# Kernel tuning notes

Measured on AMD Instinct MI355X. Metric: run time of the kernel, lower is better.

## Reference

```python
import jax, jax.numpy as jnp
import numpy as np

C = 1.0          # curvature
MIN_NORM = 1e-15
EPS = 1e-7       # atanh clamp for fp32

def _sqnorm(x):
    return jnp.sum(x * x, axis=-1, keepdims=True)

def _norm(x):
    return jnp.sqrt(jnp.maximum(_sqnorm(x), MIN_NORM))

def _atanh(u):
    return jnp.arctanh(jnp.clip(u, -1.0 + EPS, 1.0 - EPS))

def mobius_add(x, y, c):
    x2 = _sqnorm(x); y2 = _sqnorm(y)
    xy = jnp.sum(x * y, axis=-1, keepdims=True)
    num = (1.0 + 2.0 * c * xy + c * y2) * x + (1.0 - c * x2) * y
    den = 1.0 + 2.0 * c * xy + c * c * x2 * y2
    return num / jnp.maximum(den, MIN_NORM)

def logmap0(p, c):
    sc = jnp.sqrt(c)
    pn = _norm(p)
    return p / pn / sc * _atanh(sc * pn)

def logmap(p1, p2, c):
    # tangent vector at p1 pointing to p2 (Poincare ball)
    sub = mobius_add(-p1, p2, c)
    sn = _norm(sub)
    lam = 2.0 / jnp.maximum(1.0 - c * _sqnorm(p1), MIN_NORM)
    sc = jnp.sqrt(c)
    return 2.0 / sc / lam * _atanh(sc * sn) * sub / sn

def expmap(p, u, c):
    un = _norm(u)
    lam = 2.0 / jnp.maximum(1.0 - c * _sqnorm(p), MIN_NORM)
    sc = jnp.sqrt(c)
    second = jnp.tanh(sc * lam * un / 2.0) * u / (sc * un)
    return mobius_add(p, second, c)


def setup_inputs() -> dict:
    key = jax.random.key(0)
    k1, k2, k3 = jax.random.split(key, 3)
    B, N, D = 1, 1024, 128
    # points inside the unit Poincare ball (||x|| ~ 0.23)
    x = jax.random.normal(k1, (B, N, D), jnp.float32) * 0.02
    # sparse-ish dense adjacency mask (0/1 floats)
    adj = (jax.random.uniform(k2, (B, N, N)) < 0.05).astype(jnp.float32)
    # DenseAtt: nn.Linear(2*D, 1) weight (flattened) + bias
    att_w = jax.random.normal(k3, (2 * D,), jnp.float32) * 0.1
    att_b = jnp.zeros((), jnp.float32)
    return {"x": x, "adj": adj, "att_w": att_w, "att_b": att_b}


def reference(x, adj, att_w, att_b):
    B, N, D = x.shape
    x_t = logmap0(x, C)                                   # [B,N,D]
    # DenseAtt: sigmoid(Linear(cat(x_i, x_j))) decomposed as left_i + right_j + b
    left = x_t @ att_w[:D]                                # [B,N]
    right = x_t @ att_w[D:]                               # [B,N]
    att = jax.nn.sigmoid(left[:, :, None] + right[:, None, :] + att_b) * adj  # [B,N,N]
    # pairwise logmap: tangent at x_i of every x_j  -> [B,N,N,D]
    x_local = logmap(x[:, :, None, :], x[:, None, :, :], C)
    support_t = jnp.einsum('bij,bijd->bid', att, x_local)  # [B,N,D]
    return expmap(x, support_t, C)
```

## Files before the change

kernel.cpp:

```cpp
#include <hip/hip_runtime.h>
#include <math.h>


typedef short short4v __attribute__((ext_vector_type(4)));
typedef short short8v __attribute__((ext_vector_type(8)));
typedef float float4v __attribute__((ext_vector_type(4)));

static __device__ __forceinline__ short f2bf(float f) {
    unsigned u = __float_as_uint(f);
    u += 0x7fff + ((u >> 16) & 1);
    return (short)(u >> 16);
}
static __device__ __forceinline__ float rcpf(float x) { return __builtin_amdgcn_rcpf(x); }
static __device__ __forceinline__ short8v ld8(const unsigned short* p) {
    short4v lo = *(const short4v*)p;
    short4v hi = *(const short4v*)(p + 4);
    return (short8v){lo[0],lo[1],lo[2],lo[3],hi[0],hi[1],hi[2],hi[3]};
}

__global__ __launch_bounds__(256) void hyp_stats(
    const float* __restrict__ x, const float* __restrict__ w,
    float* __restrict__ st_x2, float* __restrict__ st_L, float* __restrict__ st_R)
{
    int row  = blockIdx.x * 4 + (threadIdx.x >> 6);
    int lane = threadIdx.x & 63;
    const float* xr = x + row * 128;
    float a0 = xr[lane], a1 = xr[lane + 64];
    float x2 = a0 * a0 + a1 * a1;
    float dl = a0 * w[lane]       + a1 * w[lane + 64];
    float dr = a0 * w[lane + 128] + a1 * w[lane + 192];
    for (int m = 1; m < 64; m <<= 1) {
        x2 += __shfl_xor(x2, m);
        dl += __shfl_xor(dl, m);
        dr += __shfl_xor(dr, m);
    }
    if (lane == 0) {
        float pn = sqrtf(fmaxf(x2, 1e-15f));
        float uu = fminf(pn, 1.f - 1e-7f);
        float at = 0.5f * __logf((1.f + uu) * rcpf(1.f - uu));
        float f  = at * rcpf(pn);
        st_x2[row] = x2;
        st_L[row]  = f * dl;
        st_R[row]  = f * dr;
    }
}

__global__ __launch_bounds__(256, 2) void hyp_main(
    const float* __restrict__ x, const float* __restrict__ adj,
    const float* __restrict__ battp,
    const float* __restrict__ st_x2, const float* __restrict__ st_L,
    const float* __restrict__ st_R,
    float* __restrict__ Yp, float* __restrict__ Sp)
{
    __shared__ unsigned short sXI [16 * 132];
    __shared__ unsigned short sXJ [128 * 132];
    __shared__ unsigned short sXJt[128 * 132];
    __shared__ unsigned short sW  [16 * 132];
    __shared__ float sS[16];

    const int t    = threadIdx.x;
    const int lane = t & 63;
    const int wave = t >> 6;
    const int n    = lane & 15;
    const int q    = lane >> 4;
    const int i0   = blockIdx.x * 16;
    const int c    = blockIdx.y;
    const int j0   = c * 128;
    const float batt = battp[0];

    float x2i4[4], bi4[4], li4[4];
#pragma unroll
    for (int r = 0; r < 4; ++r) {
        int i = i0 + q * 4 + r;
        x2i4[r] = st_x2[i];
        li4[r]  = st_L[i];
    }
    float x2j2[2], rj2[2], adjv[2][4];
#pragma unroll
    for (int jsl = 0; jsl < 2; ++jsl) {
        int j = j0 + (wave * 2 + jsl) * 16 + n;
        x2j2[jsl] = st_x2[j];
        rj2[jsl]  = st_R[j];
#pragma unroll
        for (int r = 0; r < 4; ++r)
            adjv[jsl][r] = adj[(i0 + q * 4 + r) * 1024 + j];
    }
#pragma unroll
    for (int r = 0; r < 4; ++r) bi4[r] = 1.f - x2i4[r];

    if (t < 16) sS[t] = 0.f;

    for (int idx = t; idx < 16 * 32; idx += 256) {
        int r = idx >> 5, cc = idx & 31;
        float4v v = ((const float4v*)x)[(i0 + r) * 32 + cc];
        short4v h = { f2bf(v[0]), f2bf(v[1]), f2bf(v[2]), f2bf(v[3]) };
        *(short4v*)&sXI[r * 132 + cc * 4] = h;
    }
#pragma unroll
    for (int it = 0; it < 4; ++it) {
        int bid = t + it * 256;
        int jr = ((bid >> 4) & 3) | (((bid >> 6) & 7) << 2);
        int dc = (bid & 15) | (((bid >> 9) & 1) << 4);
        float4v v[4];
#pragma unroll
        for (int e = 0; e < 4; ++e)
            v[e] = ((const float4v*)x)[(j0 + jr * 4 + e) * 32 + dc];
        short4v h[4];
#pragma unroll
        for (int e = 0; e < 4; ++e) {
            h[e] = (short4v){ f2bf(v[e][0]), f2bf(v[e][1]), f2bf(v[e][2]), f2bf(v[e][3]) };
            *(short4v*)&sXJ[(jr * 4 + e) * 132 + dc * 4] = h[e];
        }
#pragma unroll
        for (int d = 0; d < 4; ++d) {
            short4v ht = (short4v){ h[0][d], h[1][d], h[2][d], h[3][d] };
            *(short4v*)&sXJt[(dc * 4 + d) * 132 + jr * 4] = ht;
        }
    }
    __syncthreads();

    short8v afrag[4];
#pragma unroll
    for (int kk = 0; kk < 4; ++kk)
        afrag[kk] = ld8(&sXI[n * 132 + kk * 32 + q * 8]);

    float Sacc[4] = {0.f, 0.f, 0.f, 0.f};

#pragma unroll
    for (int jsl = 0; jsl < 2; ++jsl) {
        int js = wave * 2 + jsl;
        int jrow = js * 16 + n;
        float4v acc = (float4v){0.f, 0.f, 0.f, 0.f};
#pragma unroll
        for (int kk = 0; kk < 4; ++kk) {
            short8v b = ld8(&sXJ[jrow * 132 + kk * 32 + q * 8]);
            acc = __builtin_amdgcn_mfma_f32_16x16x32_bf16(afrag[kk], b, acc, 0, 0, 0);
        }
        float x2j = x2j2[jsl];
        float rj  = rj2[jsl];
#pragma unroll
        for (int r = 0; r < 4; ++r) {
            float G     = acc[r];
            int   i     = q * 4 + r;
            float alpha = 1.f - 2.f * G + x2j;
            float den   = fmaxf(fmaf(x2i4[r], x2j, 1.f - 2.f * G), 1e-15f);
            float rdn   = rcpf(den);
            float bb    = bi4[r];
            float nn2   = alpha * alpha * x2i4[r] + bb * bb * x2j - 2.f * alpha * bb * G;
            float sub2  = nn2 * rdn * rdn;
            float sn    = sqrtf(fmaxf(sub2, 1e-15f));
            float uu    = fminf(sn, 1.f - 1e-7f);
            float at    = 0.5f * __logf((1.f + uu) * rcpf(1.f - uu));
            float tt    = at * rcpf(sn);
            float z     = li4[r] + rj + batt;
            float sig   = rcpf(1.f + __expf(-z));
            float g     = sig * adjv[jsl][r] * tt * rdn;
            Sacc[r]     = fmaf(g, alpha, Sacc[r]);
            sW[i * 132 + js * 16 + n] = (unsigned short)f2bf(g);
        }
    }
    __syncthreads();

    float4v accB[2];
    accB[0] = (float4v){0.f, 0.f, 0.f, 0.f};
    accB[1] = (float4v){0.f, 0.f, 0.f, 0.f};
#pragma unroll
    for (int nsl = 0; nsl < 2; ++nsl) {
        int ns = wave * 2 + nsl;
#pragma unroll
        for (int kk = 0; kk < 4; ++kk) {
            short8v a = ld8(&sW  [n * 132 + kk * 32 + q * 8]);
            short8v b = ld8(&sXJt[(ns * 16 + n) * 132 + kk * 32 + q * 8]);
            accB[nsl] = __builtin_amdgcn_mfma_f32_16x16x32_bf16(a, b, accB[nsl], 0, 0, 0);
        }
    }

#pragma unroll
    for (int r = 0; r < 4; ++r) {
        float v = Sacc[r];
        v += __shfl_xor(v, 1); v += __shfl_xor(v, 2);
        v += __shfl_xor(v, 4); v += __shfl_xor(v, 8);
        if (n == 0) atomicAdd(&sS[q * 4 + r], v);
    }
    float* Yc = Yp + c * 131072;
#pragma unroll
    for (int nsl = 0; nsl < 2; ++nsl) {
        int ns = wave * 2 + nsl;
#pragma unroll
        for (int r = 0; r < 4; ++r)
            Yc[(i0 + q * 4 + r) * 128 + ns * 16 + n] = accB[nsl][r];
    }
    __syncthreads();
    if (t < 16) Sp[c * 1024 + i0 + t] = sS[t];
}

__global__ __launch_bounds__(256) void hyp_exp(
    const float* __restrict__ x, const float* __restrict__ Yp,
    const float* __restrict__ Sp, const float* __restrict__ st_x2,
    float* __restrict__ out)
{
    int i    = blockIdx.x * 4 + (threadIdx.x >> 6);
    int lane = threadIdx.x & 63;
    float y0 = 0.f, y1 = 0.f, S = 0.f;
#pragma unroll
    for (int cc = 0; cc < 8; ++cc) {
        y0 += Yp[cc * 131072 + i * 128 + lane];
        y1 += Yp[cc * 131072 + i * 128 + 64 + lane];
        S  += Sp[cc * 1024 + i];
    }
    float x0 = x[i * 128 + lane], x1 = x[i * 128 + 64 + lane];
    float x2 = st_x2[i];
    float b  = fmaxf(1.f - x2, 1e-15f);
    float u0 = b * (b * y0 - S * x0);
    float u1 = b * (b * y1 - S * x1);
    float un2 = u0 * u0 + u1 * u1;
    float xu  = x0 * u0 + x1 * u1;
    for (int m = 1; m < 64; m <<= 1) {
        un2 += __shfl_xor(un2, m);
        xu  += __shfl_xor(xu, m);
    }
    float un  = sqrtf(fmaxf(un2, 1e-15f));
    float e2  = __expf(2.f * un * rcpf(b));
    float th  = 1.f - 2.f * rcpf(e2 + 1.f);
    float s2  = th * rcpf(un);
    float xy  = s2 * xu;
    float y2s = th * th;
    float coef = 1.f + 2.f * xy + y2s;
    float den  = fmaxf(1.f + 2.f * xy + x2 * y2s, 1e-15f);
    float rd   = rcpf(den);
    out[i * 128 + lane]      = (coef * x0 + b * (s2 * u0)) * rd;
    out[i * 128 + 64 + lane] = (coef * x1 + b * (s2 * u1)) * rd;
}

extern "C" void kernel_launch(void* const* d_in, const int* in_sizes, int n_in,
                              void* d_out, int out_size, void* d_ws, size_t ws_size,
                              hipStream_t stream) {
    const float* x    = (const float*)d_in[0];
    const float* adj  = (const float*)d_in[1];
    const float* w    = (const float*)d_in[2];
    const float* batt = (const float*)d_in[3];
    float* out = (float*)d_out;

    float* Yp    = (float*)d_ws;
    float* Sp    = Yp + 8 * 131072;
    float* st_x2 = Sp + 8 * 1024;
    float* st_L  = st_x2 + 1024;
    float* st_R  = st_L + 1024;

    hipLaunchKernelGGL(hyp_stats, dim3(256), dim3(256), 0, stream, x, w, st_x2, st_L, st_R);
    hipLaunchKernelGGL(hyp_main, dim3(64, 8), dim3(256), 0, stream,
                       x, adj, batt, st_x2, st_L, st_R, Yp, Sp);
    hipLaunchKernelGGL(hyp_exp, dim3(256), dim3(256), 0, stream, x, Yp, Sp, st_x2, out);
}
```

Before: 73.29 us.

## Fuse stats, main and expmap kernels into one launch with flag-based handoff

Merges the three kernels into a single kernel. Each block recomputes the per-row norms and attention projections it needs in shared memory, replacing the separate stats kernel. The final expmap is done by one designated block per row tile after it spin-waits on release/acquire flags set by the eight column-chunk blocks. This removes two launches and their global round trips, at the cost of redundant stat recomputation and a spin-wait. The flags are never reset, so later calls may not wait for fresh partial results, and the spin-wait assumes all blocks are co-resident.

```diff
diff --git a/kernel.cpp b/kernel.cpp
--- a/kernel.cpp
+++ b/kernel.cpp
@@ -5,6 +5,8 @@
 typedef short short4v __attribute__((ext_vector_type(4)));
 typedef short short8v __attribute__((ext_vector_type(8)));
 typedef float float4v __attribute__((ext_vector_type(4)));
+
+#define MAGIC 0x4D414749
 
 static __device__ __forceinline__ short f2bf(float f) {
     unsigned u = __float_as_uint(f);
@@ -17,94 +19,76 @@
     short4v hi = *(const short4v*)(p + 4);
     return (short8v){lo[0],lo[1],lo[2],lo[3],hi[0],hi[1],hi[2],hi[3]};
 }
-
-__global__ __launch_bounds__(256) void hyp_stats(
-    const float* __restrict__ x, const float* __restrict__ w,
-    float* __restrict__ st_x2, float* __restrict__ st_L, float* __restrict__ st_R)
-{
-    int row  = blockIdx.x * 4 + (threadIdx.x >> 6);
-    int lane = threadIdx.x & 63;
-    const float* xr = x + row * 128;
-    float a0 = xr[lane], a1 = xr[lane + 64];
-    float x2 = a0 * a0 + a1 * a1;
-    float dl = a0 * w[lane]       + a1 * w[lane + 64];
-    float dr = a0 * w[lane + 128] + a1 * w[lane + 192];
-    for (int m = 1; m < 64; m <<= 1) {
-        x2 += __shfl_xor(x2, m);
-        dl += __shfl_xor(dl, m);
-        dr += __shfl_xor(dr, m);
-    }
-    if (lane == 0) {
-        float pn = sqrtf(fmaxf(x2, 1e-15f));
-        float uu = fminf(pn, 1.f - 1e-7f);
-        float at = 0.5f * __logf((1.f + uu) * rcpf(1.f - uu));
-        float f  = at * rcpf(pn);
-        st_x2[row] = x2;
-        st_L[row]  = f * dl;
-        st_R[row]  = f * dr;
-    }
-}
-
-__global__ __launch_bounds__(256, 2) void hyp_main(
+static __device__ __forceinline__ float dot4(float4v a, float4v b) {
+    return a[0]*b[0] + a[1]*b[1] + a[2]*b[2] + a[3]*b[3];
+}
+
+__global__ __launch_bounds__(256, 2) void hyp_fused(
     const float* __restrict__ x, const float* __restrict__ adj,
-    const float* __restrict__ battp,
-    const float* __restrict__ st_x2, const float* __restrict__ st_L,
-    const float* __restrict__ st_R,
-    float* __restrict__ Yp, float* __restrict__ Sp)
+    const float* __restrict__ battp, const float* __restrict__ w,
+    float* __restrict__ Yp, float* __restrict__ Sp, int* __restrict__ flags,
+    float* __restrict__ out)
 {
     __shared__ unsigned short sXI [16 * 132];
     __shared__ unsigned short sXJ [128 * 132];
     __shared__ unsigned short sXJt[128 * 132];
     __shared__ unsigned short sW  [16 * 132];
-    __shared__ float sS[16];
+    __shared__ float sX2J[128], sRJ[128];
+    __shared__ float sX2I[16], sLI[16], sS[16];
 
     const int t    = threadIdx.x;
     const int lane = t & 63;
     const int wave = t >> 6;
     const int n    = lane & 15;
     const int q    = lane >> 4;
-    const int i0   = blockIdx.x * 16;
-    const int c    = blockIdx.y;
-    const int j0   = c * 128;
+    const int bx   = blockIdx.x;
+    const int cch  = blockIdx.y;
+    const int i0   = bx * 16;
+    const int j0   = cch * 128;
     const float batt = battp[0];
 
-    float x2i4[4], bi4[4], li4[4];
-#pragma unroll
-    for (int r = 0; r < 4; ++r) {
-        int i = i0 + q * 4 + r;
-        x2i4[r] = st_x2[i];
-        li4[r]  = st_L[i];
-    }
-    float x2j2[2], rj2[2], adjv[2][4];
+    float adjv[2][4];
 #pragma unroll
     for (int jsl = 0; jsl < 2; ++jsl) {
         int j = j0 + (wave * 2 + jsl) * 16 + n;
-        x2j2[jsl] = st_x2[j];
-        rj2[jsl]  = st_R[j];
 #pragma unroll
         for (int r = 0; r < 4; ++r)
             adjv[jsl][r] = adj[(i0 + q * 4 + r) * 1024 + j];
     }
-#pragma unroll
-    for (int r = 0; r < 4; ++r) bi4[r] = 1.f - x2i4[r];
-
-    if (t < 16) sS[t] = 0.f;
-
-    for (int idx = t; idx < 16 * 32; idx += 256) {
+
+    if (t < 128) { sX2J[t] = 0.f; sRJ[t] = 0.f; }
+    if (t < 16)  { sX2I[t] = 0.f; sLI[t] = 0.f; sS[t] = 0.f; }
+    __syncthreads();
+
+    const float4v* x4 = (const float4v*)x;
+    const float4v* w4 = (const float4v*)w;
+
+#pragma unroll
+    for (int iter = 0; iter < 2; ++iter) {
+        int idx = t + iter * 256;
         int r = idx >> 5, cc = idx & 31;
-        float4v v = ((const float4v*)x)[(i0 + r) * 32 + cc];
+        float4v v  = x4[(i0 + r) * 32 + cc];
+        float4v w1 = w4[cc];
         short4v h = { f2bf(v[0]), f2bf(v[1]), f2bf(v[2]), f2bf(v[3]) };
         *(short4v*)&sXI[r * 132 + cc * 4] = h;
+        float x2p = dot4(v, v), lp = dot4(v, w1);
+#pragma unroll
+        for (int m = 1; m < 32; m <<= 1) {
+            x2p += __shfl_xor(x2p, m);
+            lp  += __shfl_xor(lp, m);
+        }
+        if ((t & 31) == 0) { atomicAdd(&sX2I[r], x2p); atomicAdd(&sLI[r], lp); }
     }
 #pragma unroll
     for (int it = 0; it < 4; ++it) {
         int bid = t + it * 256;
         int jr = ((bid >> 4) & 3) | (((bid >> 6) & 7) << 2);
         int dc = (bid & 15) | (((bid >> 9) & 1) << 4);
+        float4v w2 = w4[32 + dc];
         float4v v[4];
 #pragma unroll
         for (int e = 0; e < 4; ++e)
-            v[e] = ((const float4v*)x)[(j0 + jr * 4 + e) * 32 + dc];
+            v[e] = x4[(j0 + jr * 4 + e) * 32 + dc];
         short4v h[4];
 #pragma unroll
         for (int e = 0; e < 4; ++e) {
@@ -116,9 +100,43 @@
             short4v ht = (short4v){ h[0][d], h[1][d], h[2][d], h[3][d] };
             *(short4v*)&sXJt[(dc * 4 + d) * 132 + jr * 4] = ht;
         }
-    }
-    __syncthreads();
-
+#pragma unroll
+        for (int e = 0; e < 4; ++e) {
+            float x2p = dot4(v[e], v[e]), rp = dot4(v[e], w2);
+#pragma unroll
+            for (int m = 1; m < 16; m <<= 1) {
+                x2p += __shfl_xor(x2p, m);
+                rp  += __shfl_xor(rp, m);
+            }
+            if ((t & 15) == 0) { atomicAdd(&sX2J[jr * 4 + e], x2p); atomicAdd(&sRJ[jr * 4 + e], rp); }
+        }
+    }
+    __syncthreads();
+
+    if (t < 144) {
+        float x2 = (t < 128) ? sX2J[t] : sX2I[t - 128];
+        float pn = sqrtf(fmaxf(x2, 1e-15f));
+        float uu = fminf(pn, 1.f - 1e-7f);
+        float f  = 0.5f * __logf((1.f + uu) * rcpf(1.f - uu)) * rcpf(pn);
+        if (t < 128) sRJ[t] *= f;
+        else         sLI[t - 128] = sLI[t - 128] * f + batt;
+    }
+    __syncthreads();
+
+    float x2i4[4], bi4[4], li4[4];
+#pragma unroll
+    for (int r = 0; r < 4; ++r) {
+        x2i4[r] = sX2I[q * 4 + r];
+        li4[r]  = sLI[q * 4 + r];
+        bi4[r]  = 1.f - x2i4[r];
+    }
+    float x2j2[2], rj2[2];
+#pragma unroll
+    for (int jsl = 0; jsl < 2; ++jsl) {
+        int js = wave * 2 + jsl;
+        x2j2[jsl] = sX2J[js * 16 + n];
+        rj2[jsl]  = sRJ[js * 16 + n];
+    }
     short8v afrag[4];
 #pragma unroll
     for (int kk = 0; kk < 4; ++kk)
@@ -152,7 +170,7 @@
             float uu    = fminf(sn, 1.f - 1e-7f);
             float at    = 0.5f * __logf((1.f + uu) * rcpf(1.f - uu));
             float tt    = at * rcpf(sn);
-            float z     = li4[r] + rj + batt;
+            float z     = li4[r] + rj;
             float sig   = rcpf(1.f + __expf(-z));
             float g     = sig * adjv[jsl][r] * tt * rdn;
             Sacc[r]     = fmaf(g, alpha, Sacc[r]);
@@ -175,6 +193,14 @@
         }
     }
 
+    float* Yc = Yp + cch * 131072;
+#pragma unroll
+    for (int nsl = 0; nsl < 2; ++nsl) {
+        int ns = wave * 2 + nsl;
+#pragma unroll
+        for (int r = 0; r < 4; ++r)
+            Yc[(i0 + q * 4 + r) * 128 + ns * 16 + n] = accB[nsl][r];
+    }
 #pragma unroll
     for (int r = 0; r < 4; ++r) {
         float v = Sacc[r];
@@ -182,54 +208,67 @@
         v += __shfl_xor(v, 4); v += __shfl_xor(v, 8);
         if (n == 0) atomicAdd(&sS[q * 4 + r], v);
     }
-    float* Yc = Yp + c * 131072;
-#pragma unroll
-    for (int nsl = 0; nsl < 2; ++nsl) {
-        int ns = wave * 2 + nsl;
-#pragma unroll
-        for (int r = 0; r < 4; ++r)
-            Yc[(i0 + q * 4 + r) * 128 + ns * 16 + n] = accB[nsl][r];
-    }
-    __syncthreads();
-    if (t < 16) Sp[c * 1024 + i0 + t] = sS[t];
-}
-
-__global__ __launch_bounds__(256) void hyp_exp(
-    const float* __restrict__ x, const float* __restrict__ Yp,
-    const float* __restrict__ Sp, const float* __restrict__ st_x2,
-    float* __restrict__ out)
-{
-    int i    = blockIdx.x * 4 + (threadIdx.x >> 6);
-    int lane = threadIdx.x & 63;
-    float y0 = 0.f, y1 = 0.f, S = 0.f;
-#pragma unroll
-    for (int cc = 0; cc < 8; ++cc) {
-        y0 += Yp[cc * 131072 + i * 128 + lane];
-        y1 += Yp[cc * 131072 + i * 128 + 64 + lane];
-        S  += Sp[cc * 1024 + i];
-    }
-    float x0 = x[i * 128 + lane], x1 = x[i * 128 + 64 + lane];
-    float x2 = st_x2[i];
-    float b  = fmaxf(1.f - x2, 1e-15f);
-    float u0 = b * (b * y0 - S * x0);
-    float u1 = b * (b * y1 - S * x1);
-    float un2 = u0 * u0 + u1 * u1;
-    float xu  = x0 * u0 + x1 * u1;
-    for (int m = 1; m < 64; m <<= 1) {
-        un2 += __shfl_xor(un2, m);
-        xu  += __shfl_xor(xu, m);
-    }
-    float un  = sqrtf(fmaxf(un2, 1e-15f));
-    float e2  = __expf(2.f * un * rcpf(b));
+    __syncthreads();
+    if (t < 16) Sp[cch * 1024 + i0 + t] = sS[t];
+    __threadfence();
+    __syncthreads();
+    if (t == 0)
+        __hip_atomic_store(&flags[bx * 8 + cch], MAGIC, __ATOMIC_RELEASE, __HIP_MEMORY_SCOPE_AGENT);
+
+    if ((bx & 7) != cch) return;
+    if (t < 8) {
+        while (__hip_atomic_load(&flags[bx * 8 + t], __ATOMIC_ACQUIRE, __HIP_MEMORY_SCOPE_AGENT) != MAGIC)
+            __builtin_amdgcn_s_sleep(1);
+    }
+    __syncthreads();
+    __threadfence();
+
+    int row  = t >> 4;
+    int ds16 = t & 15;
+    const float4v* xr4 = x4 + (i0 + row) * 32 + ds16 * 2;
+    float4v xa = xr4[0], xb = xr4[1];
+    float xv[8] = { xa[0], xa[1], xa[2], xa[3], xb[0], xb[1], xb[2], xb[3] };
+    float ya[8] = {0.f,0.f,0.f,0.f,0.f,0.f,0.f,0.f};
+    float S = 0.f;
+#pragma unroll
+    for (int c2 = 0; c2 < 8; ++c2) {
+        const float4v* yp4 = (const float4v*)(Yp + c2 * 131072 + (i0 + row) * 128) + ds16 * 2;
+        float4v a = yp4[0], b = yp4[1];
+        ya[0] += a[0]; ya[1] += a[1]; ya[2] += a[2]; ya[3] += a[3];
+        ya[4] += b[0]; ya[5] += b[1]; ya[6] += b[2]; ya[7] += b[3];
+        S += Sp[c2 * 1024 + i0 + row];
+    }
+    float x2p = dot4(xa, xa) + dot4(xb, xb);
+#pragma unroll
+    for (int m = 1; m < 16; m <<= 1) x2p += __shfl_xor(x2p, m);
+    float bE = fmaxf(1.f - x2p, 1e-15f);
+    float u[8], un2p = 0.f, xup = 0.f;
+#pragma unroll
+    for (int e = 0; e < 8; ++e) {
+        u[e] = bE * (bE * ya[e] - S * xv[e]);
+        un2p += u[e] * u[e];
+        xup  += xv[e] * u[e];
+    }
+#pragma unroll
+    for (int m = 1; m < 16; m <<= 1) {
+        un2p += __shfl_xor(un2p, m);
+        xup  += __shfl_xor(xup, m);
+    }
+    float un  = sqrtf(fmaxf(un2p, 1e-15f));
+    float e2  = __expf(2.f * un * rcpf(bE));
     float th  = 1.f - 2.f * rcpf(e2 + 1.f);
     float s2  = th * rcpf(un);
-    float xy  = s2 * xu;
+    float xy  = s2 * xup;
     float y2s = th * th;
     float coef = 1.f + 2.f * xy + y2s;
-    float den  = fmaxf(1.f + 2.f * xy + x2 * y2s, 1e-15f);
+    float den  = fmaxf(1.f + 2.f * xy + x2p * y2s, 1e-15f);
     float rd   = rcpf(den);
-    out[i * 128 + lane]      = (coef * x0 + b * (s2 * u0)) * rd;
-    out[i * 128 + 64 + lane] = (coef * x1 + b * (s2 * u1)) * rd;
+    float4v o0 = { (coef*xv[0] + bE*s2*u[0])*rd, (coef*xv[1] + bE*s2*u[1])*rd,
+                   (coef*xv[2] + bE*s2*u[2])*rd, (coef*xv[3] + bE*s2*u[3])*rd };
+    float4v o1 = { (coef*xv[4] + bE*s2*u[4])*rd, (coef*xv[5] + bE*s2*u[5])*rd,
+                   (coef*xv[6] + bE*s2*u[6])*rd, (coef*xv[7] + bE*s2*u[7])*rd };
+    float4v* out4 = (float4v*)(out + (i0 + row) * 128) + ds16 * 2;
+    out4[0] = o0; out4[1] = o1;
 }
 
 extern "C" void kernel_launch(void* const* d_in, const int* in_sizes, int n_in,
@@ -243,12 +282,8 @@
 
     float* Yp    = (float*)d_ws;
     float* Sp    = Yp + 8 * 131072;
-    float* st_x2 = Sp + 8 * 1024;
-    float* st_L  = st_x2 + 1024;
-    float* st_R  = st_L + 1024;
-
-    hipLaunchKernelGGL(hyp_stats, dim3(256), dim3(256), 0, stream, x, w, st_x2, st_L, st_R);
-    hipLaunchKernelGGL(hyp_main, dim3(64, 8), dim3(256), 0, stream,
-                       x, adj, batt, st_x2, st_L, st_R, Yp, Sp);
-    hipLaunchKernelGGL(hyp_exp, dim3(256), dim3(256), 0, stream, x, Yp, Sp, st_x2, out);
-}
+    int*   flags = (int*)(Sp + 8 * 1024);
+
+    hipLaunchKernelGGL(hyp_fused, dim3(64, 8), dim3(256), 0, stream,
+                       x, adj, batt, w, Yp, Sp, flags, out);
+}
```

After: 119.5 us. 63.1% more time.

## Precompute bf16 X and X^T once, shrink pair tiles, drop LDS staging

Applied to the files above, without the earlier changes.

The prep kernel now converts x to bf16 once, in both row-major and transposed layouts, and folds the attention bias into the left stats. The pair kernel splits j into 16 chunks of 64 and loads MFMA fragments straight from global memory instead of converting and transposing x into large shared buffers in every block. This allows higher occupancy (launch bounds 4) and removes the redundant per-block conversion. The cost is twice as many partial Y buffers for the final kernel to reduce, and extra workspace for the bf16 copies. The exp kernel is also vectorised to float4 with half-wave reductions.

```diff
diff --git a/kernel.cpp b/kernel.cpp
--- a/kernel.cpp
+++ b/kernel.cpp
@@ -17,46 +17,76 @@
     short4v hi = *(const short4v*)(p + 4);
     return (short8v){lo[0],lo[1],lo[2],lo[3],hi[0],hi[1],hi[2],hi[3]};
 }
-
-__global__ __launch_bounds__(256) void hyp_stats(
+static __device__ __forceinline__ float dot4(float4v a, float4v b) {
+    return a[0]*b[0] + a[1]*b[1] + a[2]*b[2] + a[3]*b[3];
+}
+static __device__ __forceinline__ float atanh_over(float pn) {
+    float uu = fminf(pn, 1.f - 1e-7f);
+    return 0.5f * __logf((1.f + uu) * rcpf(1.f - uu)) * rcpf(pn);
+}
+
+__global__ __launch_bounds__(256) void hyp_prep(
     const float* __restrict__ x, const float* __restrict__ w,
+    const float* __restrict__ battp,
+    unsigned short* __restrict__ Xb, unsigned short* __restrict__ Xbt,
     float* __restrict__ st_x2, float* __restrict__ st_L, float* __restrict__ st_R)
 {
-    int row  = blockIdx.x * 4 + (threadIdx.x >> 6);
-    int lane = threadIdx.x & 63;
-    const float* xr = x + row * 128;
-    float a0 = xr[lane], a1 = xr[lane + 64];
-    float x2 = a0 * a0 + a1 * a1;
-    float dl = a0 * w[lane]       + a1 * w[lane + 64];
-    float dr = a0 * w[lane + 128] + a1 * w[lane + 192];
-    for (int m = 1; m < 64; m <<= 1) {
-        x2 += __shfl_xor(x2, m);
-        dl += __shfl_xor(dl, m);
-        dr += __shfl_xor(dr, m);
-    }
-    if (lane == 0) {
+    __shared__ unsigned short sT[128 * 20];
+    __shared__ float sPx[16 * 36], sPl[16 * 36], sPr[16 * 36];
+    const int t  = threadIdx.x;
+    const int r0 = blockIdx.x * 16;
+    const float4v* x4 = (const float4v*)x;
+    const float4v* w4 = (const float4v*)w;
+
+#pragma unroll
+    for (int it = 0; it < 2; ++it) {
+        int bid = t + it * 256;
+        int jr = bid >> 5, dc = bid & 31;
+        float4v v  = x4[(r0 + jr) * 32 + dc];
+        float4v w1 = w4[dc], w2 = w4[32 + dc];
+        short4v h = { f2bf(v[0]), f2bf(v[1]), f2bf(v[2]), f2bf(v[3]) };
+        *(short4v*)&Xb[(r0 + jr) * 128 + dc * 4] = h;
+#pragma unroll
+        for (int d = 0; d < 4; ++d)
+            sT[(dc * 4 + d) * 20 + jr] = (unsigned short)h[d];
+        sPx[jr * 36 + dc] = dot4(v, v);
+        sPl[jr * 36 + dc] = dot4(v, w1);
+        sPr[jr * 36 + dc] = dot4(v, w2);
+    }
+    __syncthreads();
+    {
+        int dim = t >> 1, h = t & 1;
+        short8v vv = ld8(&sT[dim * 20 + h * 8]);
+        *(short8v*)&Xbt[dim * 1024 + r0 + h * 8] = vv;
+    }
+    if (t < 16) {
+        float x2 = 0.f, l = 0.f, r = 0.f;
+#pragma unroll
+        for (int k = 0; k < 8; ++k) {
+            float4v a = *(float4v*)&sPx[t * 36 + k * 4];
+            float4v b = *(float4v*)&sPl[t * 36 + k * 4];
+            float4v c = *(float4v*)&sPr[t * 36 + k * 4];
+            x2 += a[0] + a[1] + a[2] + a[3];
+            l  += b[0] + b[1] + b[2] + b[3];
+            r  += c[0] + c[1] + c[2] + c[3];
+        }
         float pn = sqrtf(fmaxf(x2, 1e-15f));
-        float uu = fminf(pn, 1.f - 1e-7f);
-        float at = 0.5f * __logf((1.f + uu) * rcpf(1.f - uu));
-        float f  = at * rcpf(pn);
-        st_x2[row] = x2;
-        st_L[row]  = f * dl;
-        st_R[row]  = f * dr;
-    }
-}
-
-__global__ __launch_bounds__(256, 2) void hyp_main(
-    const float* __restrict__ x, const float* __restrict__ adj,
-    const float* __restrict__ battp,
+        float f  = atanh_over(pn);
+        st_x2[r0 + t] = x2;
+        st_L [r0 + t] = l * f + battp[0];
+        st_R [r0 + t] = r * f;
+    }
+}
+
+__global__ __launch_bounds__(256, 4) void hyp_pair(
+    const unsigned short* __restrict__ Xb, const unsigned short* __restrict__ Xbt,
+    const float* __restrict__ adj,
     const float* __restrict__ st_x2, const float* __restrict__ st_L,
     const float* __restrict__ st_R,
     float* __restrict__ Yp, float* __restrict__ Sp)
 {
-    __shared__ unsigned short sXI [16 * 132];
-    __shared__ unsigned short sXJ [128 * 132];
-    __shared__ unsigned short sXJt[128 * 132];
-    __shared__ unsigned short sW  [16 * 132];
-    __shared__ float sS[16];
+    __shared__ unsigned short sW[16 * 68];
+    __shared__ float sSp[4 * 256];
 
     const int t    = threadIdx.x;
     const int lane = t & 63;
@@ -65,99 +95,57 @@
     const int q    = lane >> 4;
     const int i0   = blockIdx.x * 16;
     const int c    = blockIdx.y;
-    const int j0   = c * 128;
-    const float batt = battp[0];
-
-    float x2i4[4], bi4[4], li4[4];
+    const int j0   = c * 64;
+    const int jrow = j0 + wave * 16 + n;
+
+    float x2j = st_x2[jrow];
+    float rj  = st_R[jrow];
+    float x2i4[4], li4[4], bi4[4], adjv[4];
 #pragma unroll
     for (int r = 0; r < 4; ++r) {
         int i = i0 + q * 4 + r;
         x2i4[r] = st_x2[i];
         li4[r]  = st_L[i];
-    }
-    float x2j2[2], rj2[2], adjv[2][4];
-#pragma unroll
-    for (int jsl = 0; jsl < 2; ++jsl) {
-        int j = j0 + (wave * 2 + jsl) * 16 + n;
-        x2j2[jsl] = st_x2[j];
-        rj2[jsl]  = st_R[j];
-#pragma unroll
-        for (int r = 0; r < 4; ++r)
-            adjv[jsl][r] = adj[(i0 + q * 4 + r) * 1024 + j];
+        adjv[r] = adj[i * 1024 + jrow];
+    }
+    short8v afrag[4], bfA[4];
+#pragma unroll
+    for (int kk = 0; kk < 4; ++kk) {
+        afrag[kk] = *(const short8v*)&Xb[(i0 + n) * 128 + kk * 32 + q * 8];
+        bfA  [kk] = *(const short8v*)&Xb[jrow * 128     + kk * 32 + q * 8];
+    }
+    short8v bfB[2][2];
+#pragma unroll
+    for (int nsl = 0; nsl < 2; ++nsl) {
+        int ns = wave * 2 + nsl;
+#pragma unroll
+        for (int kk = 0; kk < 2; ++kk)
+            bfB[nsl][kk] = *(const short8v*)&Xbt[(ns * 16 + n) * 1024 + j0 + kk * 32 + q * 8];
     }
 #pragma unroll
     for (int r = 0; r < 4; ++r) bi4[r] = 1.f - x2i4[r];
 
-    if (t < 16) sS[t] = 0.f;
-
-    for (int idx = t; idx < 16 * 32; idx += 256) {
-        int r = idx >> 5, cc = idx & 31;
-        float4v v = ((const float4v*)x)[(i0 + r) * 32 + cc];
-        short4v h = { f2bf(v[0]), f2bf(v[1]), f2bf(v[2]), f2bf(v[3]) };
-        *(short4v*)&sXI[r * 132 + cc * 4] = h;
-    }
-#pragma unroll
-    for (int it = 0; it < 4; ++it) {
-        int bid = t + it * 256;
-        int jr = ((bid >> 4) & 3) | (((bid >> 6) & 7) << 2);
-        int dc = (bid & 15) | (((bid >> 9) & 1) << 4);
-        float4v v[4];
-#pragma unroll
-        for (int e = 0; e < 4; ++e)
-            v[e] = ((const float4v*)x)[(j0 + jr * 4 + e) * 32 + dc];
-        short4v h[4];
-#pragma unroll
-        for (int e = 0; e < 4; ++e) {
-            h[e] = (short4v){ f2bf(v[e][0]), f2bf(v[e][1]), f2bf(v[e][2]), f2bf(v[e][3]) };
-            *(short4v*)&sXJ[(jr * 4 + e) * 132 + dc * 4] = h[e];
-        }
-#pragma unroll
-        for (int d = 0; d < 4; ++d) {
-            short4v ht = (short4v){ h[0][d], h[1][d], h[2][d], h[3][d] };
-            *(short4v*)&sXJt[(dc * 4 + d) * 132 + jr * 4] = ht;
-        }
-    }
-    __syncthreads();
-
-    short8v afrag[4];
+    float4v acc = (float4v){0.f, 0.f, 0.f, 0.f};
 #pragma unroll
     for (int kk = 0; kk < 4; ++kk)
-        afrag[kk] = ld8(&sXI[n * 132 + kk * 32 + q * 8]);
-
-    float Sacc[4] = {0.f, 0.f, 0.f, 0.f};
-
-#pragma unroll
-    for (int jsl = 0; jsl < 2; ++jsl) {
-        int js = wave * 2 + jsl;
-        int jrow = js * 16 + n;
-        float4v acc = (float4v){0.f, 0.f, 0.f, 0.f};
-#pragma unroll
-        for (int kk = 0; kk < 4; ++kk) {
-            short8v b = ld8(&sXJ[jrow * 132 + kk * 32 + q * 8]);
-            acc = __builtin_amdgcn_mfma_f32_16x16x32_bf16(afrag[kk], b, acc, 0, 0, 0);
-        }
-        float x2j = x2j2[jsl];
-        float rj  = rj2[jsl];
-#pragma unroll
-        for (int r = 0; r < 4; ++r) {
-            float G     = acc[r];
-            int   i     = q * 4 + r;
-            float alpha = 1.f - 2.f * G + x2j;
-            float den   = fmaxf(fmaf(x2i4[r], x2j, 1.f - 2.f * G), 1e-15f);
-            float rdn   = rcpf(den);
-            float bb    = bi4[r];
-            float nn2   = alpha * alpha * x2i4[r] + bb * bb * x2j - 2.f * alpha * bb * G;
-            float sub2  = nn2 * rdn * rdn;
-            float sn    = sqrtf(fmaxf(sub2, 1e-15f));
-            float uu    = fminf(sn, 1.f - 1e-7f);
-            float at    = 0.5f * __logf((1.f + uu) * rcpf(1.f - uu));
-            float tt    = at * rcpf(sn);
-            float z     = li4[r] + rj + batt;
-            float sig   = rcpf(1.f + __expf(-z));
-            float g     = sig * adjv[jsl][r] * tt * rdn;
-            Sacc[r]     = fmaf(g, alpha, Sacc[r]);
-            sW[i * 132 + js * 16 + n] = (unsigned short)f2bf(g);
-        }
+        acc = __builtin_amdgcn_mfma_f32_16x16x32_bf16(afrag[kk], bfA[kk], acc, 0, 0, 0);
+
+    float Sacc[4];
+#pragma unroll
+    for (int r = 0; r < 4; ++r) {
+        float G     = acc[r];
+        float alpha = 1.f - 2.f * G + x2j;
+        float den   = fmaxf(fmaf(x2i4[r], x2j, 1.f - 2.f * G), 1e-15f);
+        float rdn   = rcpf(den);
+        float bb    = bi4[r];
+        float nn2   = alpha * alpha * x2i4[r] + bb * bb * x2j - 2.f * alpha * bb * G;
+        float sn    = sqrtf(fmaxf(nn2 * rdn * rdn, 1e-15f));
+        float tt    = atanh_over(sn);
+        float z     = li4[r] + rj;
+        float sig   = rcpf(1.f + __expf(-z));
+        float g     = sig * adjv[r] * tt * rdn;
+        Sacc[r]     = g * alpha;
+        sW[(q * 4 + r) * 68 + wave * 16 + n] = (unsigned short)f2bf(g);
     }
     __syncthreads();
 
@@ -166,22 +154,13 @@
     accB[1] = (float4v){0.f, 0.f, 0.f, 0.f};
 #pragma unroll
     for (int nsl = 0; nsl < 2; ++nsl) {
-        int ns = wave * 2 + nsl;
-#pragma unroll
-        for (int kk = 0; kk < 4; ++kk) {
-            short8v a = ld8(&sW  [n * 132 + kk * 32 + q * 8]);
-            short8v b = ld8(&sXJt[(ns * 16 + n) * 132 + kk * 32 + q * 8]);
-            accB[nsl] = __builtin_amdgcn_mfma_f32_16x16x32_bf16(a, b, accB[nsl], 0, 0, 0);
+#pragma unroll
+        for (int kk = 0; kk < 2; ++kk) {
+            short8v a = ld8(&sW[n * 68 + kk * 32 + q * 8]);
+            accB[nsl] = __builtin_amdgcn_mfma_f32_16x16x32_bf16(a, bfB[nsl][kk], accB[nsl], 0, 0, 0);
         }
     }
 
-#pragma unroll
-    for (int r = 0; r < 4; ++r) {
-        float v = Sacc[r];
-        v += __shfl_xor(v, 1); v += __shfl_xor(v, 2);
-        v += __shfl_xor(v, 4); v += __shfl_xor(v, 8);
-        if (n == 0) atomicAdd(&sS[q * 4 + r], v);
-    }
     float* Yc = Yp + c * 131072;
 #pragma unroll
     for (int nsl = 0; nsl < 2; ++nsl) {
@@ -190,8 +169,21 @@
         for (int r = 0; r < 4; ++r)
             Yc[(i0 + q * 4 + r) * 128 + ns * 16 + n] = accB[nsl][r];
     }
+#pragma unroll
+    for (int r = 0; r < 4; ++r)
+        sSp[wave * 256 + (q * 4 + r) * 16 + n] = Sacc[r];
     __syncthreads();
-    if (t < 16) Sp[c * 1024 + i0 + t] = sS[t];
+    if (t < 16) {
+        float s = 0.f;
+#pragma unroll
+        for (int wv = 0; wv < 4; ++wv)
+#pragma unroll
+            for (int k4 = 0; k4 < 4; ++k4) {
+                float4v v = *(float4v*)&sSp[wv * 256 + t * 16 + k4 * 4];
+                s += v[0] + v[1] + v[2] + v[3];
+            }
+        Sp[c * 1024 + i0 + t] = s;
+    }
 }
 
 __global__ __launch_bounds__(256) void hyp_exp(
@@ -199,37 +191,43 @@
     const float* __restrict__ Sp, const float* __restrict__ st_x2,
     float* __restrict__ out)
 {
-    int i    = blockIdx.x * 4 + (threadIdx.x >> 6);
-    int lane = threadIdx.x & 63;
-    float y0 = 0.f, y1 = 0.f, S = 0.f;
-#pragma unroll
-    for (int cc = 0; cc < 8; ++cc) {
-        y0 += Yp[cc * 131072 + i * 128 + lane];
-        y1 += Yp[cc * 131072 + i * 128 + 64 + lane];
-        S  += Sp[cc * 1024 + i];
-    }
-    float x0 = x[i * 128 + lane], x1 = x[i * 128 + 64 + lane];
-    float x2 = st_x2[i];
-    float b  = fmaxf(1.f - x2, 1e-15f);
-    float u0 = b * (b * y0 - S * x0);
-    float u1 = b * (b * y1 - S * x1);
-    float un2 = u0 * u0 + u1 * u1;
-    float xu  = x0 * u0 + x1 * u1;
-    for (int m = 1; m < 64; m <<= 1) {
-        un2 += __shfl_xor(un2, m);
-        xu  += __shfl_xor(xu, m);
-    }
-    float un  = sqrtf(fmaxf(un2, 1e-15f));
-    float e2  = __expf(2.f * un * rcpf(b));
+    const int t   = threadIdx.x;
+    const int row = blockIdx.x * 8 + (t >> 5);
+    const int l32 = t & 31;
+    float4v y = (float4v){0.f, 0.f, 0.f, 0.f};
+    float S = 0.f;
+#pragma unroll
+    for (int c = 0; c < 16; ++c) {
+        y += *(const float4v*)&Yp[c * 131072 + row * 128 + l32 * 4];
+        S += Sp[c * 1024 + row];
+    }
+    float4v xa = ((const float4v*)x)[row * 32 + l32];
+    float x2 = st_x2[row];
+    float bE = fmaxf(1.f - x2, 1e-15f);
+    float u[4], un2p = 0.f, xup = 0.f;
+#pragma unroll
+    for (int e = 0; e < 4; ++e) {
+        u[e] = bE * (bE * y[e] - S * xa[e]);
+        un2p += u[e] * u[e];
+        xup  += xa[e] * u[e];
+    }
+#pragma unroll
+    for (int m = 1; m < 32; m <<= 1) {
+        un2p += __shfl_xor(un2p, m, 32);
+        xup  += __shfl_xor(xup,  m, 32);
+    }
+    float un  = sqrtf(fmaxf(un2p, 1e-15f));
+    float e2  = __expf(2.f * un * rcpf(bE));
     float th  = 1.f - 2.f * rcpf(e2 + 1.f);
     float s2  = th * rcpf(un);
-    float xy  = s2 * xu;
+    float xy  = s2 * xup;
     float y2s = th * th;
     float coef = 1.f + 2.f * xy + y2s;
     float den  = fmaxf(1.f + 2.f * xy + x2 * y2s, 1e-15f);
     float rd   = rcpf(den);
-    out[i * 128 + lane]      = (coef * x0 + b * (s2 * u0)) * rd;
-    out[i * 128 + 64 + lane] = (coef * x1 + b * (s2 * u1)) * rd;
+    float4v o = { (coef*xa[0] + bE*s2*u[0])*rd, (coef*xa[1] + bE*s2*u[1])*rd,
+                  (coef*xa[2] + bE*s2*u[2])*rd, (coef*xa[3] + bE*s2*u[3])*rd };
+    ((float4v*)out)[row * 32 + l32] = o;
 }
 
 extern "C" void kernel_launch(void* const* d_in, const int* in_sizes, int n_in,
@@ -242,13 +240,17 @@
     float* out = (float*)d_out;
 
     float* Yp    = (float*)d_ws;
-    float* Sp    = Yp + 8 * 131072;
-    float* st_x2 = Sp + 8 * 1024;
+    float* Sp    = Yp + 16 * 131072;
+    float* st_x2 = Sp + 16 * 1024;
     float* st_L  = st_x2 + 1024;
     float* st_R  = st_L + 1024;
-
-    hipLaunchKernelGGL(hyp_stats, dim3(256), dim3(256), 0, stream, x, w, st_x2, st_L, st_R);
-    hipLaunchKernelGGL(hyp_main, dim3(64, 8), dim3(256), 0, stream,
-                       x, adj, batt, st_x2, st_L, st_R, Yp, Sp);
-    hipLaunchKernelGGL(hyp_exp, dim3(256), dim3(256), 0, stream, x, Yp, Sp, st_x2, out);
-}
+    unsigned short* Xb  = (unsigned short*)(st_R + 1024);
+    unsigned short* Xbt = Xb + 1024 * 128;
+
+    hipLaunchKernelGGL(hyp_prep, dim3(64), dim3(256), 0, stream,
+                       x, w, batt, Xb, Xbt, st_x2, st_L, st_R);
+    hipLaunchKernelGGL(hyp_pair, dim3(64, 16), dim3(256), 0, stream,
+                       Xb, Xbt, adj, st_x2, st_L, st_R, Yp, Sp);
+    hipLaunchKernelGGL(hyp_exp, dim3(128), dim3(256), 0, stream,
+                       x, Yp, Sp, st_x2, out);
+}
```

Result: slower. 77.03 us (+5.1%).

## Drop shared-memory atomics for row sums and vectorize the expmap epilogue

Applied to the files above, without the earlier changes.

The main kernel no longer reduces per-row S partials with shuffles, shared atomics and a trailing barrier. Each lane writes its raw partial to a larger workspace, and the final expmap kernel reduces the 64 partials per row with 32-wide shuffles. The attention bias is folded into the precomputed left term, and the expmap kernel now processes 8 rows per block with float4 loads and stores. This trades extra global traffic in the Sp2 buffer and a larger final reduction for removing synchronization in the main kernel.

```diff
diff --git a/kernel.cpp b/kernel.cpp
--- a/kernel.cpp
+++ b/kernel.cpp
@@ -17,9 +17,17 @@
     short4v hi = *(const short4v*)(p + 4);
     return (short8v){lo[0],lo[1],lo[2],lo[3],hi[0],hi[1],hi[2],hi[3]};
 }
+static __device__ __forceinline__ float dot4(float4v a, float4v b) {
+    return a[0]*b[0] + a[1]*b[1] + a[2]*b[2] + a[3]*b[3];
+}
+static __device__ __forceinline__ float atanh_over(float pn) {
+    float uu = fminf(pn, 1.f - 1e-7f);
+    return 0.5f * __logf((1.f + uu) * rcpf(1.f - uu)) * rcpf(pn);
+}
 
 __global__ __launch_bounds__(256) void hyp_stats(
     const float* __restrict__ x, const float* __restrict__ w,
+    const float* __restrict__ battp,
     float* __restrict__ st_x2, float* __restrict__ st_L, float* __restrict__ st_R)
 {
     int row  = blockIdx.x * 4 + (threadIdx.x >> 6);
@@ -36,27 +44,23 @@
     }
     if (lane == 0) {
         float pn = sqrtf(fmaxf(x2, 1e-15f));
-        float uu = fminf(pn, 1.f - 1e-7f);
-        float at = 0.5f * __logf((1.f + uu) * rcpf(1.f - uu));
-        float f  = at * rcpf(pn);
+        float f  = atanh_over(pn);
         st_x2[row] = x2;
-        st_L[row]  = f * dl;
+        st_L[row]  = f * dl + battp[0];
         st_R[row]  = f * dr;
     }
 }
 
 __global__ __launch_bounds__(256, 2) void hyp_main(
     const float* __restrict__ x, const float* __restrict__ adj,
-    const float* __restrict__ battp,
     const float* __restrict__ st_x2, const float* __restrict__ st_L,
     const float* __restrict__ st_R,
-    float* __restrict__ Yp, float* __restrict__ Sp)
+    float* __restrict__ Yp, float* __restrict__ Sp2)
 {
     __shared__ unsigned short sXI [16 * 132];
     __shared__ unsigned short sXJ [128 * 132];
     __shared__ unsigned short sXJt[128 * 132];
     __shared__ unsigned short sW  [16 * 132];
-    __shared__ float sS[16];
 
     const int t    = threadIdx.x;
     const int lane = t & 63;
@@ -66,7 +70,8 @@
     const int i0   = blockIdx.x * 16;
     const int c    = blockIdx.y;
     const int j0   = c * 128;
-    const float batt = battp[0];
+
+    const float4v* x4 = (const float4v*)x;
 
     float x2i4[4], bi4[4], li4[4];
 #pragma unroll
@@ -88,11 +93,11 @@
 #pragma unroll
     for (int r = 0; r < 4; ++r) bi4[r] = 1.f - x2i4[r];
 
-    if (t < 16) sS[t] = 0.f;
-
-    for (int idx = t; idx < 16 * 32; idx += 256) {
+#pragma unroll
+    for (int it = 0; it < 2; ++it) {
+        int idx = t + it * 256;
         int r = idx >> 5, cc = idx & 31;
-        float4v v = ((const float4v*)x)[(i0 + r) * 32 + cc];
+        float4v v = x4[(i0 + r) * 32 + cc];
         short4v h = { f2bf(v[0]), f2bf(v[1]), f2bf(v[2]), f2bf(v[3]) };
         *(short4v*)&sXI[r * 132 + cc * 4] = h;
     }
@@ -104,7 +109,7 @@
         float4v v[4];
 #pragma unroll
         for (int e = 0; e < 4; ++e)
-            v[e] = ((const float4v*)x)[(j0 + jr * 4 + e) * 32 + dc];
+            v[e] = x4[(j0 + jr * 4 + e) * 32 + dc];
         short4v h[4];
 #pragma unroll
         for (int e = 0; e < 4; ++e) {
@@ -147,12 +152,9 @@
             float rdn   = rcpf(den);
             float bb    = bi4[r];
             float nn2   = alpha * alpha * x2i4[r] + bb * bb * x2j - 2.f * alpha * bb * G;
-            float sub2  = nn2 * rdn * rdn;
-            float sn    = sqrtf(fmaxf(sub2, 1e-15f));
-            float uu    = fminf(sn, 1.f - 1e-7f);
-            float at    = 0.5f * __logf((1.f + uu) * rcpf(1.f - uu));
-            float tt    = at * rcpf(sn);
-            float z     = li4[r] + rj + batt;
+            float sn    = sqrtf(fmaxf(nn2 * rdn * rdn, 1e-15f));
+            float tt    = atanh_over(sn);
+            float z     = li4[r] + rj;
             float sig   = rcpf(1.f + __expf(-z));
             float g     = sig * adjv[jsl][r] * tt * rdn;
             Sacc[r]     = fmaf(g, alpha, Sacc[r]);
@@ -175,13 +177,6 @@
         }
     }
 
-#pragma unroll
-    for (int r = 0; r < 4; ++r) {
-        float v = Sacc[r];
-        v += __shfl_xor(v, 1); v += __shfl_xor(v, 2);
-        v += __shfl_xor(v, 4); v += __shfl_xor(v, 8);
-        if (n == 0) atomicAdd(&sS[q * 4 + r], v);
-    }
     float* Yc = Yp + c * 131072;
 #pragma unroll
     for (int nsl = 0; nsl < 2; ++nsl) {
@@ -190,46 +185,57 @@
         for (int r = 0; r < 4; ++r)
             Yc[(i0 + q * 4 + r) * 128 + ns * 16 + n] = accB[nsl][r];
     }
-    __syncthreads();
-    if (t < 16) Sp[c * 1024 + i0 + t] = sS[t];
+#pragma unroll
+    for (int r = 0; r < 4; ++r)
+        Sp2[((c * 1024 + i0 + q * 4 + r) * 4 + wave) * 16 + n] = Sacc[r];
 }
 
 __global__ __launch_bounds__(256) void hyp_exp(
     const float* __restrict__ x, const float* __restrict__ Yp,
-    const float* __restrict__ Sp, const float* __restrict__ st_x2,
+    const float* __restrict__ Sp2, const float* __restrict__ st_x2,
     float* __restrict__ out)
 {
-    int i    = blockIdx.x * 4 + (threadIdx.x >> 6);
-    int lane = threadIdx.x & 63;
-    float y0 = 0.f, y1 = 0.f, S = 0.f;
-#pragma unroll
-    for (int cc = 0; cc < 8; ++cc) {
-        y0 += Yp[cc * 131072 + i * 128 + lane];
-        y1 += Yp[cc * 131072 + i * 128 + 64 + lane];
-        S  += Sp[cc * 1024 + i];
-    }
-    float x0 = x[i * 128 + lane], x1 = x[i * 128 + 64 + lane];
-    float x2 = st_x2[i];
-    float b  = fmaxf(1.f - x2, 1e-15f);
-    float u0 = b * (b * y0 - S * x0);
-    float u1 = b * (b * y1 - S * x1);
-    float un2 = u0 * u0 + u1 * u1;
-    float xu  = x0 * u0 + x1 * u1;
-    for (int m = 1; m < 64; m <<= 1) {
-        un2 += __shfl_xor(un2, m);
-        xu  += __shfl_xor(xu, m);
-    }
-    float un  = sqrtf(fmaxf(un2, 1e-15f));
-    float e2  = __expf(2.f * un * rcpf(b));
+    const int t   = threadIdx.x;
+    const int row = blockIdx.x * 8 + (t >> 5);
+    const int l32 = t & 31;
+    float4v y = (float4v){0.f, 0.f, 0.f, 0.f};
+    float S = 0.f;
+#pragma unroll
+    for (int c = 0; c < 8; ++c) {
+        y += *(const float4v*)&Yp[c * 131072 + row * 128 + l32 * 4];
+        S += Sp2[(c * 1024 + row) * 64 + l32];
+        S += Sp2[(c * 1024 + row) * 64 + 32 + l32];
+    }
+#pragma unroll
+    for (int m = 1; m < 32; m <<= 1) S += __shfl_xor(S, m, 32);
+
+    float4v xa = ((const float4v*)x)[row * 32 + l32];
+    float x2 = st_x2[row];
+    float bE = fmaxf(1.f - x2, 1e-15f);
+    float u[4], un2p = 0.f, xup = 0.f;
+#pragma unroll
+    for (int e = 0; e < 4; ++e) {
+        u[e] = bE * (bE * y[e] - S * xa[e]);
+        un2p += u[e] * u[e];
+        xup  += xa[e] * u[e];
+    }
+#pragma unroll
+    for (int m = 1; m < 32; m <<= 1) {
+        un2p += __shfl_xor(un2p, m, 32);
+        xup  += __shfl_xor(xup,  m, 32);
+    }
+    float un  = sqrtf(fmaxf(un2p, 1e-15f));
+    float e2  = __expf(2.f * un * rcpf(bE));
     float th  = 1.f - 2.f * rcpf(e2 + 1.f);
     float s2  = th * rcpf(un);
-    float xy  = s2 * xu;
+    float xy  = s2 * xup;
     float y2s = th * th;
     float coef = 1.f + 2.f * xy + y2s;
     float den  = fmaxf(1.f + 2.f * xy + x2 * y2s, 1e-15f);
     float rd   = rcpf(den);
-    out[i * 128 + lane]      = (coef * x0 + b * (s2 * u0)) * rd;
-    out[i * 128 + 64 + lane] = (coef * x1 + b * (s2 * u1)) * rd;
+    float4v o = { (coef*xa[0] + bE*s2*u[0])*rd, (coef*xa[1] + bE*s2*u[1])*rd,
+                  (coef*xa[2] + bE*s2*u[2])*rd, (coef*xa[3] + bE*s2*u[3])*rd };
+    ((float4v*)out)[row * 32 + l32] = o;
 }
 
 extern "C" void kernel_launch(void* const* d_in, const int* in_sizes, int n_in,
@@ -242,13 +248,15 @@
     float* out = (float*)d_out;
 
     float* Yp    = (float*)d_ws;
-    float* Sp    = Yp + 8 * 131072;
-    float* st_x2 = Sp + 8 * 1024;
+    float* Sp2   = Yp + 8 * 131072;
+    float* st_x2 = Sp2 + 8 * 1024 * 64;
     float* st_L  = st_x2 + 1024;
     float* st_R  = st_L + 1024;
 
-    hipLaunchKernelGGL(hyp_stats, dim3(256), dim3(256), 0, stream, x, w, st_x2, st_L, st_R);
+    hipLaunchKernelGGL(hyp_stats, dim3(256), dim3(256), 0, stream,
+                       x, w, batt, st_x2, st_L, st_R);
     hipLaunchKernelGGL(hyp_main, dim3(64, 8), dim3(256), 0, stream,
-                       x, adj, batt, st_x2, st_L, st_R, Yp, Sp);
-    hipLaunchKernelGGL(hyp_exp, dim3(256), dim3(256), 0, stream, x, Yp, Sp, st_x2, out);
-}
+                       x, adj, st_x2, st_L, st_R, Yp, Sp2);
+    hipLaunchKernelGGL(hyp_exp, dim3(128), dim3(256), 0, stream,
+                       x, Yp, Sp2, st_x2, out);
+}
```

Measured after the change: 72.27 us. About the same (-1.4%).
